# Optimization experiments

Hardware: AMD Instinct MI355X
Metric: run time of the kernel (lower is better)

## Reference

```python
import jax, jax.numpy as jnp
import numpy as np

LAMB_LABELS = 1.0
LAMB_BBOXES = 5.0
LAMB_GENIOU = 2.0


def box_cxcywh_to_xyxy(x):
    cx, cy, w, h = x[..., 0], x[..., 1], x[..., 2], x[..., 3]
    return jnp.stack([cx - 0.5 * w, cy - 0.5 * h, cx + 0.5 * w, cy + 0.5 * h], axis=-1)


def generalized_box_iou(b1, b2):
    # b1: [P,4] xyxy, b2: [T,4] xyxy -> [P,T] pairwise GIoU
    area1 = (b1[:, 2] - b1[:, 0]) * (b1[:, 3] - b1[:, 1])
    area2 = (b2[:, 2] - b2[:, 0]) * (b2[:, 3] - b2[:, 1])
    lt = jnp.maximum(b1[:, None, :2], b2[None, :, :2])
    rb = jnp.minimum(b1[:, None, 2:], b2[None, :, 2:])
    wh = jnp.clip(rb - lt, 0.0)
    inter = wh[..., 0] * wh[..., 1]
    union = area1[:, None] + area2[None, :] - inter
    iou = inter / union
    lt_e = jnp.minimum(b1[:, None, :2], b2[None, :, :2])
    rb_e = jnp.maximum(b1[:, None, 2:], b2[None, :, 2:])
    wh_e = jnp.clip(rb_e - lt_e, 0.0)
    area_e = wh_e[..., 0] * wh_e[..., 1]
    return iou - (area_e - union) / area_e


def setup_inputs() -> dict:
    key = jax.random.key(0)
    k1, k2, k3, k4 = jax.random.split(key, 4)
    B, N, C, T = 16, 900, 92, 960
    out_labels = jax.random.normal(k1, (B, N, C), dtype=jnp.float32)
    out_bboxes = jax.random.uniform(k2, (B, N, 4), dtype=jnp.float32)
    tgt_labels = jax.random.randint(k3, (T,), 0, C, dtype=jnp.int64)
    tgt_bboxes = jax.random.uniform(k4, (T, 4), dtype=jnp.float32)
    return {"out_labels": out_labels, "out_bboxes": out_bboxes,
            "tgt_labels": tgt_labels, "tgt_bboxes": tgt_bboxes}


def reference(out_labels, out_bboxes, tgt_labels, tgt_bboxes):
    B, N, C = out_labels.shape
    # '(b n) d' softmax over classes, then gather target-label columns
    probs = jax.nn.softmax(out_labels.reshape(B * N, C), axis=-1)
    cost_labels = 1.0 - probs[:, tgt_labels]                     # [BN, T]
    ob = out_bboxes.reshape(B * N, 4)
    # pairwise L1 (torch.cdist p=1)
    cost_bboxes = jnp.sum(jnp.abs(ob[:, None, :] - tgt_bboxes[None, :, :]), axis=-1)
    # NOTE: original converts only predicted boxes to xyxy (targets used as-is)
    cost_geniou = 1.0 - generalized_box_iou(box_cxcywh_to_xyxy(ob), tgt_bboxes)
    cost = (LAMB_LABELS * cost_labels + LAMB_BBOXES * cost_bboxes
            + LAMB_GENIOU * cost_geniou)
    return cost.reshape(B, N, -1)                                # [B, N, T]
```

## Files before the change

kernel.cpp:

```cpp
#include <hip/hip_runtime.h>
#include <math.h>

constexpr int kB = 16, kN = 900, kC = 92, kT = 960;
constexpr int kBN = kB * kN;
constexpr int ROWS = 4;
constexpr int THREADS = 256;

__global__ __launch_bounds__(THREADS) void matcher_kernel(
    const float* __restrict__ out_labels,
    const float* __restrict__ out_bboxes,
    const int*   __restrict__ tgt_labels,
    const float* __restrict__ tgt_bboxes,
    float*       __restrict__ cost)
{
    __shared__ float4 s_tb[kT];
    __shared__ int    s_lab[kT];
    __shared__ float  s_probs[ROWS][kC];
    __shared__ float  s_row[ROWS][12];

    const int tid  = threadIdx.x;
    const int row0 = blockIdx.x * ROWS;

    const float4* tb4 = (const float4*)tgt_bboxes;
    for (int i = tid; i < kT; i += THREADS) {
        s_tb[i]  = tb4[i];
        s_lab[i] = tgt_labels[i];
    }

    {
        const int wave = tid >> 6;
        const int lane = tid & 63;
        const int r = wave;
        const int p = row0 + r;
        const float* lrow = out_labels + (size_t)p * kC;
        float x0 = (lane < kC)      ? lrow[lane]      : -INFINITY;
        float x1 = (lane + 64 < kC) ? lrow[lane + 64] : -INFINITY;
        float m = fmaxf(x0, x1);
        #pragma unroll
        for (int off = 32; off > 0; off >>= 1)
            m = fmaxf(m, __shfl_down(m, off, 64));
        m = __shfl(m, 0, 64);
        float e0 = (lane < kC)      ? expf(x0 - m) : 0.0f;
        float e1 = (lane + 64 < kC) ? expf(x1 - m) : 0.0f;
        float s = e0 + e1;
        #pragma unroll
        for (int off = 32; off > 0; off >>= 1)
            s += __shfl_down(s, off, 64);
        s = __shfl(s, 0, 64);
        float inv = 1.0f / s;
        if (lane < kC)      s_probs[r][lane]      = e0 * inv;
        if (lane + 64 < kC) s_probs[r][lane + 64] = e1 * inv;
        if (lane == 0) {
            float4 bb = ((const float4*)out_bboxes)[p];
            float hw = 0.5f * bb.z, hh = 0.5f * bb.w;
            float bx0 = bb.x - hw, by0 = bb.y - hh;
            float bx1 = bb.x + hw, by1 = bb.y + hh;
            s_row[r][0] = bb.x; s_row[r][1] = bb.y;
            s_row[r][2] = bb.z; s_row[r][3] = bb.w;
            s_row[r][4] = bx0;  s_row[r][5] = by0;
            s_row[r][6] = bx1;  s_row[r][7] = by1;
            s_row[r][8] = (bx1 - bx0) * (by1 - by0);
        }
    }
    __syncthreads();

    for (int r = 0; r < ROWS; ++r) {
        const int p = row0 + r;
        const float cx = s_row[r][0], cy = s_row[r][1];
        const float w  = s_row[r][2], h  = s_row[r][3];
        const float bx0 = s_row[r][4], by0 = s_row[r][5];
        const float bx1 = s_row[r][6], by1 = s_row[r][7];
        const float area1 = s_row[r][8];
        float* orow = cost + (size_t)p * kT;
        for (int t = tid; t < kT; t += THREADS) {
            float4 tb = s_tb[t];
            float l1 = fabsf(cx - tb.x) + fabsf(cy - tb.y)
                     + fabsf(w  - tb.z) + fabsf(h  - tb.w);
            float ltx = fmaxf(bx0, tb.x), lty = fmaxf(by0, tb.y);
            float rbx = fminf(bx1, tb.z), rby = fminf(by1, tb.w);
            float iw = fmaxf(rbx - ltx, 0.0f), ih = fmaxf(rby - lty, 0.0f);
            float inter = iw * ih;
            float area2 = (tb.z - tb.x) * (tb.w - tb.y);
            float uni = area1 + area2 - inter;
            float iou = inter / uni;
            float ex0 = fminf(bx0, tb.x), ey0 = fminf(by0, tb.y);
            float ex1 = fmaxf(bx1, tb.z), ey1 = fmaxf(by1, tb.w);
            float ew = fmaxf(ex1 - ex0, 0.0f), eh = fmaxf(ey1 - ey0, 0.0f);
            float area_e = ew * eh;
            float giou = iou - (area_e - uni) / area_e;
            float cl = 1.0f - s_probs[r][s_lab[t]];
            orow[t] = cl + 5.0f * l1 + 2.0f * (1.0f - giou);
        }
    }
}

extern "C" void kernel_launch(void* const* d_in, const int* in_sizes, int n_in,
                              void* d_out, int out_size, void* d_ws, size_t ws_size,
                              hipStream_t stream) {
    const float* out_labels = (const float*)d_in[0];
    const float* out_bboxes = (const float*)d_in[1];
    const int*   tgt_labels = (const int*)d_in[2];
    const float* tgt_bboxes = (const float*)d_in[3];
    float* cost = (float*)d_out;
    dim3 grid(kBN / ROWS);
    matcher_kernel<<<grid, THREADS, 0, stream>>>(out_labels, out_bboxes,
                                                 tgt_labels, tgt_bboxes, cost);
}
```

Baseline: 99.66 us.

## Vectorize cost stores to float4 and fold GIoU algebra with fast reciprocals

Each thread now handles four consecutive targets across all rows, so target boxes, areas and labels are loaded once and reused, and outputs go out as float4 stores. The cost expression is rewritten algebraically: constants are folded into the stored class term (5 - p), the redundant clip on the enclosing box is dropped, and the two divisions become hardware reciprocal approximations. Exact IEEE division is traded for the rcp instruction, which may change low-order bits. Only 240 of the 256 threads now do output work.

Measured after the change: 91.57 us. 8.1% less time.

```diff
diff --git a/kernel.cpp b/kernel.cpp
--- a/kernel.cpp
+++ b/kernel.cpp
@@ -15,8 +15,10 @@
 {
     __shared__ float4 s_tb[kT];
     __shared__ int    s_lab[kT];
-    __shared__ float  s_probs[ROWS][kC];
-    __shared__ float  s_row[ROWS][12];
+    __shared__ float  s_cl[ROWS][kC];
+    __shared__ float4 s_rowA[ROWS];
+    __shared__ float4 s_rowB[ROWS];
+    __shared__ float  s_rowC[ROWS];
 
     const int tid  = threadIdx.x;
     const int row0 = blockIdx.x * ROWS;
@@ -28,9 +30,8 @@
     }
 
     {
-        const int wave = tid >> 6;
+        const int r = tid >> 6;
         const int lane = tid & 63;
-        const int r = wave;
         const int p = row0 + r;
         const float* lrow = out_labels + (size_t)p * kC;
         float x0 = (lane < kC)      ? lrow[lane]      : -INFINITY;
@@ -48,48 +49,59 @@
             s += __shfl_down(s, off, 64);
         s = __shfl(s, 0, 64);
         float inv = 1.0f / s;
-        if (lane < kC)      s_probs[r][lane]      = e0 * inv;
-        if (lane + 64 < kC) s_probs[r][lane + 64] = e1 * inv;
+        if (lane < kC)      s_cl[r][lane]      = 5.0f - e0 * inv;
+        if (lane + 64 < kC) s_cl[r][lane + 64] = 5.0f - e1 * inv;
         if (lane == 0) {
             float4 bb = ((const float4*)out_bboxes)[p];
             float hw = 0.5f * bb.z, hh = 0.5f * bb.w;
             float bx0 = bb.x - hw, by0 = bb.y - hh;
             float bx1 = bb.x + hw, by1 = bb.y + hh;
-            s_row[r][0] = bb.x; s_row[r][1] = bb.y;
-            s_row[r][2] = bb.z; s_row[r][3] = bb.w;
-            s_row[r][4] = bx0;  s_row[r][5] = by0;
-            s_row[r][6] = bx1;  s_row[r][7] = by1;
-            s_row[r][8] = (bx1 - bx0) * (by1 - by0);
+            s_rowA[r] = bb;
+            s_rowB[r] = make_float4(bx0, by0, bx1, by1);
+            s_rowC[r] = (bx1 - bx0) * (by1 - by0);
         }
     }
     __syncthreads();
 
-    for (int r = 0; r < ROWS; ++r) {
-        const int p = row0 + r;
-        const float cx = s_row[r][0], cy = s_row[r][1];
-        const float w  = s_row[r][2], h  = s_row[r][3];
-        const float bx0 = s_row[r][4], by0 = s_row[r][5];
-        const float bx1 = s_row[r][6], by1 = s_row[r][7];
-        const float area1 = s_row[r][8];
-        float* orow = cost + (size_t)p * kT;
-        for (int t = tid; t < kT; t += THREADS) {
-            float4 tb = s_tb[t];
-            float l1 = fabsf(cx - tb.x) + fabsf(cy - tb.y)
-                     + fabsf(w  - tb.z) + fabsf(h  - tb.w);
-            float ltx = fmaxf(bx0, tb.x), lty = fmaxf(by0, tb.y);
-            float rbx = fminf(bx1, tb.z), rby = fminf(by1, tb.w);
-            float iw = fmaxf(rbx - ltx, 0.0f), ih = fmaxf(rby - lty, 0.0f);
-            float inter = iw * ih;
-            float area2 = (tb.z - tb.x) * (tb.w - tb.y);
-            float uni = area1 + area2 - inter;
-            float iou = inter / uni;
-            float ex0 = fminf(bx0, tb.x), ey0 = fminf(by0, tb.y);
-            float ex1 = fmaxf(bx1, tb.z), ey1 = fmaxf(by1, tb.w);
-            float ew = fmaxf(ex1 - ex0, 0.0f), eh = fmaxf(ey1 - ey0, 0.0f);
-            float area_e = ew * eh;
-            float giou = iou - (area_e - uni) / area_e;
-            float cl = 1.0f - s_probs[r][s_lab[t]];
-            orow[t] = cl + 5.0f * l1 + 2.0f * (1.0f - giou);
+    const int t0 = tid * 4;
+    if (t0 < kT) {
+        float4 tb[4]; float a2[4]; int li[4];
+        #pragma unroll
+        for (int i = 0; i < 4; ++i) {
+            tb[i] = s_tb[t0 + i];
+            a2[i] = (tb[i].z - tb[i].x) * (tb[i].w - tb[i].y);
+            li[i] = s_lab[t0 + i];
+        }
+        #pragma unroll
+        for (int r = 0; r < ROWS; ++r) {
+            const int p = row0 + r;
+            float4 ra = s_rowA[r];
+            float4 rb = s_rowB[r];
+            float area1 = s_rowC[r];
+            float4 res;
+            float* resp = &res.x;
+            #pragma unroll
+            for (int i = 0; i < 4; ++i) {
+                float4 t = tb[i];
+                float l1 = fabsf(ra.x - t.x) + fabsf(ra.y - t.y)
+                         + fabsf(ra.z - t.z) + fabsf(ra.w - t.w);
+                float ltx = fmaxf(rb.x, t.x), lty = fmaxf(rb.y, t.y);
+                float rbx = fminf(rb.z, t.z), rby = fminf(rb.w, t.w);
+                float iw = fmaxf(rbx - ltx, 0.0f), ih = fmaxf(rby - lty, 0.0f);
+                float inter = iw * ih;
+                float uni = area1 + a2[i] - inter;
+                float ex0 = fminf(rb.x, t.x), ey0 = fminf(rb.y, t.y);
+                float ex1 = fmaxf(rb.z, t.z), ey1 = fmaxf(rb.w, t.w);
+                float area_e = (ex1 - ex0) * (ey1 - ey0);
+                float rcpu = __builtin_amdgcn_rcpf(uni);
+                float rcpe = __builtin_amdgcn_rcpf(area_e);
+                float v = s_cl[r][li[i]];
+                v = fmaf(5.0f, l1, v);
+                v = fmaf(-2.0f * inter, rcpu, v);
+                v = fmaf(-2.0f * uni, rcpe, v);
+                resp[i] = v;
+            }
+            ((float4*)(cost + (size_t)p * kT))[tid] = res;
         }
     }
 }
```
